# Kernel tuning notes

Measured on AMD Instinct MI355X. Metric: run time of the kernel, lower is better.

## Reference

```python
import jax, jax.numpy as jnp
import numpy as np

DIM = 512
D_IN = 4096
N_OBJ = 2048
N_REL = 32768
STEPS = 2
N_OBJ_CLS = 151
N_REL_CLS = 51
EPS = 1e-5


def _mlp2(x, w1, b1, w2, b2):
    # Linear -> ReLU -> Linear (torch Linear: y = x W^T + b)
    return jnp.maximum(x @ w1.T + b1, 0.0) @ w2.T + b2


def _gate(a, b, w, bias):
    # Sequential(Linear(2*dim, 1), Sigmoid) on cat([a, b], 1)
    return jax.nn.sigmoid(jnp.concatenate([a, b], axis=1) @ w.T + bias)


def _gru_cell(x, h, wih, whh, bih, bhh):
    gi = x @ wih.T + bih  # [N, 3*DIM]
    gh = h @ whh.T + bhh
    ir, iz, inew = jnp.split(gi, 3, axis=1)
    hr, hz, hnew = jnp.split(gh, 3, axis=1)
    r = jax.nn.sigmoid(ir + hr)
    z = jax.nn.sigmoid(iz + hz)
    n = jnp.tanh(inew + r * hnew)
    return (1.0 - z) * n + z * h


def setup_inputs() -> dict:
    key = jax.random.key(0)
    ks = jax.random.split(key, 32)
    rn = lambda k, shape, s=0.02: jax.random.normal(k, shape, dtype=jnp.float32) * s
    z = lambda *shape: jnp.zeros(shape, dtype=jnp.float32)
    return {
        'x_obj': jax.random.normal(ks[0], (N_OBJ, D_IN), dtype=jnp.float32),
        'x_pred': jax.random.normal(ks[1], (N_REL, D_IN), dtype=jnp.float32),
        'rel_inds': jax.random.randint(ks[2], (N_REL, 2), 0, N_OBJ),
        # obj / pred embedding MLPs
        'oe_w1': rn(ks[3], (DIM, D_IN)), 'oe_b1': z(DIM),
        'oe_w2': rn(ks[4], (DIM, DIM)), 'oe_b2': z(DIM),
        'pe_w1': rn(ks[5], (DIM, D_IN)), 'pe_b1': z(DIM),
        'pe_w2': rn(ks[6], (DIM, DIM)), 'pe_b2': z(DIM),
        # gates: Linear(2*dim, 1)
        'g_sn_w': rn(ks[7], (1, 2 * DIM)), 'g_sn_b': z(1),
        'g_on_w': rn(ks[8], (1, 2 * DIM)), 'g_on_b': z(1),
        'g_se_w': rn(ks[9], (1, 2 * DIM)), 'g_se_b': z(1),
        'g_oe_w': rn(ks[10], (1, 2 * DIM)), 'g_oe_b': z(1),
        # GRU cells
        'ngru_wih': rn(ks[11], (3 * DIM, DIM)), 'ngru_whh': rn(ks[12], (3 * DIM, DIM)),
        'ngru_bih': z(3 * DIM), 'ngru_bhh': z(3 * DIM),
        'egru_wih': rn(ks[13], (3 * DIM, DIM)), 'egru_whh': rn(ks[14], (3 * DIM, DIM)),
        'egru_bih': z(3 * DIM), 'egru_bhh': z(3 * DIM),
        # classifier heads
        'op_w': rn(ks[15], (N_OBJ_CLS, DIM)), 'op_b': z(N_OBJ_CLS),
        'pp_w': rn(ks[16], (N_REL_CLS, DIM)), 'pp_b': z(N_REL_CLS),
    }


def reference(x_obj, x_pred, rel_inds,
              oe_w1, oe_b1, oe_w2, oe_b2,
              pe_w1, pe_b1, pe_w2, pe_b2,
              g_sn_w, g_sn_b, g_on_w, g_on_b,
              g_se_w, g_se_b, g_oe_w, g_oe_b,
              ngru_wih, ngru_whh, ngru_bih, ngru_bhh,
              egru_wih, egru_whh, egru_bih, egru_bhh,
              op_w, op_b, pp_w, pp_b):
    n_obj = x_obj.shape[0]
    subj_idx = rel_inds[:, 0]
    obj_idx = rel_inds[:, 1]

    h_obj = _mlp2(x_obj, oe_w1, oe_b1, oe_w2, oe_b2)    # [N_obj, DIM]
    h_edge = _mlp2(x_pred, pe_w1, pe_b1, pe_w2, pe_b2)  # [N_rel, DIM]

    # row sums of the 0/1 subj/obj_pred_map == in-degree counts (constants)
    ones = jnp.ones((rel_inds.shape[0],), dtype=jnp.float32)
    cnt_s = jax.ops.segment_sum(ones, subj_idx, num_segments=n_obj)[:, None]
    cnt_o = jax.ops.segment_sum(ones, obj_idx, num_segments=n_obj)[:, None]

    for _ in range(STEPS):
        sub_vert = h_obj[subj_idx]  # [N_rel, DIM]
        obj_vert = h_obj[obj_idx]

        # node update: gated edge->node messages, mean-aggregated per node
        msg_p2s = _gate(sub_vert, h_edge, g_sn_w, g_sn_b) * h_edge
        msg_p2o = _gate(obj_vert, h_edge, g_on_w, g_on_b) * h_edge
        node_message = (
            jax.ops.segment_sum(msg_p2s, subj_idx, num_segments=n_obj) / (cnt_s + EPS)
            + jax.ops.segment_sum(msg_p2o, obj_idx, num_segments=n_obj) / (cnt_o + EPS)
        ) / 2.0
        new_h_obj = _gru_cell(node_message, h_obj, ngru_wih, ngru_whh, ngru_bih, ngru_bhh)

        # edge update: gated node->edge messages
        msg_s2p = _gate(sub_vert, h_edge, g_se_w, g_se_b) * sub_vert
        msg_o2p = _gate(obj_vert, h_edge, g_oe_w, g_oe_b) * obj_vert
        edge_message = (msg_s2p + msg_o2p) / 2.0
        h_edge = _gru_cell(edge_message, h_edge, egru_wih, egru_whh, egru_bih, egru_bhh)
        h_obj = new_h_obj

    obj_class_logits = h_obj @ op_w.T + op_b    # [N_obj, 151]
    pred_class_logits = h_edge @ pp_w.T + pp_b  # [N_rel, 51]
    obj_class_labels = jnp.argmax(obj_class_logits[:, 1:], axis=1) + 1
    return (h_obj, h_edge, obj_class_logits, pred_class_logits, obj_class_labels, rel_inds)
```

## Files before the change

kernel.cpp:

```cpp
#include <hip/hip_runtime.h>
#include <math.h>

typedef unsigned short u16;
typedef unsigned int u32;
typedef _Float16 f16;
typedef f16 f16x8 __attribute__((ext_vector_type(8)));
typedef float f32x4 __attribute__((ext_vector_type(4)));

#define DIM 512
#define D_IN 4096
#define N_OBJS 2048
#define N_RELS 32768
#define N_OBJ_CLS 151
#define N_REL_CLS 51
#define EPSV 1e-5f

#define OFF_HOBJ  0
#define OFF_HEDGE (N_OBJS*DIM)
#define OFF_OLOG  (OFF_HEDGE + N_RELS*DIM)
#define OFF_PLOG  (OFF_OLOG + N_OBJS*N_OBJ_CLS)
#define OFF_LBL   (OFF_PLOG + N_RELS*N_REL_CLS)
#define OFF_RI    (OFF_LBL + N_OBJS)

__device__ __forceinline__ float sigmoidf_(float x) { return 1.0f / (1.0f + expf(-x)); }
__device__ __forceinline__ u16 f2h_(float f) {
    union { f16 h; u16 u; } c; c.h = (f16)f; return c.u;
}
__device__ __forceinline__ float h2f_(u16 u) {
    union { f16 h; u16 u; } c; c.u = u; return (float)c.h;
}

__device__ __forceinline__ void cvt8h1(const float* f, uint4& h) {
    u32 hh[8];
#pragma unroll
    for (int i = 0; i < 8; i++) hh[i] = f2h_(f[i]);
    h.x = hh[0] | (hh[1] << 16); h.y = hh[2] | (hh[3] << 16);
    h.z = hh[4] | (hh[5] << 16); h.w = hh[6] | (hh[7] << 16);
}
__device__ __forceinline__ void cvt8h2(const float* f, uint4& h, uint4& l) {
    u32 hh[8], ll[8];
#pragma unroll
    for (int i = 0; i < 8; i++) {
        u16 x = f2h_(f[i]);
        hh[i] = x;
        ll[i] = f2h_(f[i] - h2f_(x));
    }
    h.x = hh[0] | (hh[1] << 16); h.y = hh[2] | (hh[3] << 16);
    h.z = hh[4] | (hh[5] << 16); h.w = hh[6] | (hh[7] << 16);
    l.x = ll[0] | (ll[1] << 16); l.y = ll[2] | (ll[3] << 16);
    l.z = ll[4] | (ll[5] << 16); l.w = ll[6] | (ll[7] << 16);
}

__device__ __forceinline__ int swzo(int row, int c) {
    return row * 32 + ((c ^ ((row >> 1) & 3)) << 3);
}

__device__ __forceinline__ int xcdswz(int orig, int nwg) {
    const int q = nwg >> 3;
    return (orig & 7) * q + (orig >> 3);
}

__device__ __forceinline__ void gload16(const void* g, void* l) {
    __builtin_amdgcn_global_load_lds(
        (const __attribute__((address_space(1))) void*)g,
        (__attribute__((address_space(3))) void*)l, 16, 0, 0);
}

__global__ __launch_bounds__(256) void convert_h(const float* __restrict__ src,
    u16* __restrict__ hi, int n4)
{
    const int i = blockIdx.x * 256 + threadIdx.x;
    if (i >= n4) return;
    const float4 v = ((const float4*)src)[i];
    ((ushort4*)hi)[i] = make_ushort4(f2h_(v.x), f2h_(v.y), f2h_(v.z), f2h_(v.w));
}

template<bool RELU, int AT, bool WSPLIT>
__global__ __launch_bounds__(256, 3) void gemm_a32(
    const float* __restrict__ A, const u16* __restrict__ Bhi,
    const float* __restrict__ bias, u16* __restrict__ Chi, u16* __restrict__ Clo,
    int NX, int K)
{
    __shared__ u16 sAh[128 * 32], sBh[128 * 32];
    __shared__ u16 sAl[AT == 2 ? 128 * 32 : 1];
    const int id = xcdswz(blockIdx.x, gridDim.x);
    const int m0 = (id / NX) * 128, n0 = (id % NX) * 128;
    const int N = NX * 128;
    const int t = threadIdx.x;
    const int wid = t >> 6, lane = t & 63;
    const int wm = (wid >> 1) * 64, wn = (wid & 1) * 64;
    const int lr = lane & 15, lk = lane >> 4;

    f32x4 acc[4][4] = {};

    const int sr = t >> 1;
    const int sc = (t & 1) * 2;
    const float* Ap = A + (size_t)(m0 + sr) * K + (t & 1) * 16;

    const int rB = (wid * 2) * 16 + (lane >> 2);
    const int cB = (lane & 3) ^ ((rB >> 1) & 3);
    const u16* Bp0 = Bhi + (size_t)(n0 + rB) * K + cB * 8;
    const u16* Bp1 = Bp0 + (size_t)16 * K;
    u16* Bd0 = &sBh[(wid * 2) * 512];
    u16* Bd1 = Bd0 + 512;

    float fv[16];
    *(float4*)&fv[0]  = *(const float4*)(Ap);
    *(float4*)&fv[4]  = *(const float4*)(Ap + 4);
    *(float4*)&fv[8]  = *(const float4*)(Ap + 8);
    *(float4*)&fv[12] = *(const float4*)(Ap + 12);

    for (int k0 = 0; k0 < K; k0 += 32) {
        uint4 ah0, ah1, al0, al1;
        if (AT == 2) { cvt8h2(fv, ah0, al0); cvt8h2(fv + 8, ah1, al1); }
        else         { cvt8h1(fv, ah0);      cvt8h1(fv + 8, ah1); }

        __syncthreads();
        gload16(Bp0 + k0, Bd0);
        gload16(Bp1 + k0, Bd1);
        *(uint4*)&sAh[swzo(sr, sc)]     = ah0;
        *(uint4*)&sAh[swzo(sr, sc + 1)] = ah1;
        if (AT == 2) {
            *(uint4*)&sAl[swzo(sr, sc)]     = al0;
            *(uint4*)&sAl[swzo(sr, sc + 1)] = al1;
        }
        asm volatile("s_waitcnt vmcnt(0)" ::: "memory");
        __syncthreads();

        const int kn = k0 + 32;
        if (kn < K) {
            *(float4*)&fv[0]  = *(const float4*)(Ap + kn);
            *(float4*)&fv[4]  = *(const float4*)(Ap + kn + 4);
            *(float4*)&fv[8]  = *(const float4*)(Ap + kn + 8);
            *(float4*)&fv[12] = *(const float4*)(Ap + kn + 12);
        }

        f16x8 ah[4], al[4], bh[4];
#pragma unroll
        for (int f = 0; f < 4; f++) {
            const int off = swzo(wm + f * 16 + lr, lk);
            ah[f] = *(const f16x8*)&sAh[off];
            if (AT == 2) al[f] = *(const f16x8*)&sAl[off];
            bh[f] = *(const f16x8*)&sBh[swzo(wn + f * 16 + lr, lk)];
        }
#pragma unroll
        for (int fm = 0; fm < 4; fm++)
#pragma unroll
            for (int fn = 0; fn < 4; fn++) {
                acc[fm][fn] = __builtin_amdgcn_mfma_f32_16x16x32_f16(ah[fm], bh[fn], acc[fm][fn], 0, 0, 0);
                if (AT == 2)
                    acc[fm][fn] = __builtin_amdgcn_mfma_f32_16x16x32_f16(al[fm], bh[fn], acc[fm][fn], 0, 0, 0);
            }
    }
#pragma unroll
    for (int fm = 0; fm < 4; fm++) {
        const int mrow = m0 + wm + fm * 16 + lk * 4;
#pragma unroll
        for (int fn = 0; fn < 4; fn++) {
            const int col = n0 + wn + fn * 16 + lr;
            const float bv = bias[col];
#pragma unroll
            for (int j = 0; j < 4; j++) {
                float v = acc[fm][fn][j] + bv;
                if (RELU) v = fmaxf(v, 0.0f);
                const u16 h = f2h_(v);
                Chi[(size_t)(mrow + j) * N + col] = h;
                if (WSPLIT) Clo[(size_t)(mrow + j) * N + col] = f2h_(v - h2f_(h));
            }
        }
    }
}

template<int AT, bool WF32, bool WHI, bool WLO>
__global__ __launch_bounds__(256, AT == 1 ? 4 : 3) void gemm_f16(
    const u16* __restrict__ Ahi, const u16* __restrict__ Alo,
    const u16* __restrict__ Bhi, const float* __restrict__ bias,
    float* __restrict__ C32, u16* __restrict__ Chi, u16* __restrict__ Clo,
    int NX, int N, int ldc, int K)
{
    __shared__ u16 sA[2][128 * 32], sB[2][128 * 32];
    __shared__ u16 sL[AT == 2 ? 2 : 1][AT == 2 ? 128 * 32 : 1];
    const int id = xcdswz(blockIdx.x, gridDim.x);
    const int m0 = (id / NX) * 128, n0 = (id % NX) * 128;
    const int t = threadIdx.x;
    const int wid = t >> 6, lane = t & 63;
    const int wm = (wid >> 1) * 64, wn = (wid & 1) * 64;
    const int lr = lane & 15, lk = lane >> 4;

    f32x4 acc[4][4] = {};

    const int rr = (wid * 2) * 16 + (lane >> 2);
    const int cc = (lane & 3) ^ ((rr >> 1) & 3);
    const u16* pA0 = Ahi + (size_t)(m0 + rr) * K + cc * 8;
    const u16* pA1 = pA0 + (size_t)16 * K;
    const u16* pL0 = (AT == 2) ? Alo + (size_t)(m0 + rr) * K + cc * 8 : nullptr;
    const u16* pL1 = (AT == 2) ? pL0 + (size_t)16 * K : nullptr;
    const u16* pB0 = Bhi + (size_t)(n0 + rr) * K + cc * 8;
    const u16* pB1 = pB0 + (size_t)16 * K;
    const int bOff = (wid * 2) * 512;

    for (int k0 = 0; k0 < K; k0 += 64) {
        __syncthreads();
#pragma unroll
        for (int h = 0; h < 2; h++) {
            const int kk = k0 + h * 32;
            gload16(pA0 + kk, &sA[h][bOff]);
            gload16(pA1 + kk, &sA[h][bOff + 512]);
            if (AT == 2) {
                gload16(pL0 + kk, &sL[h][bOff]);
                gload16(pL1 + kk, &sL[h][bOff + 512]);
            }
            gload16(pB0 + kk, &sB[h][bOff]);
            gload16(pB1 + kk, &sB[h][bOff + 512]);
        }
        asm volatile("s_waitcnt vmcnt(0)" ::: "memory");
        __syncthreads();

#pragma unroll
        for (int h = 0; h < 2; h++) {
            f16x8 ah[4], al[4], bh[4];
#pragma unroll
            for (int f = 0; f < 4; f++) {
                const int off = swzo(wm + f * 16 + lr, lk);
                ah[f] = *(const f16x8*)&sA[h][off];
                if (AT == 2) al[f] = *(const f16x8*)&sL[h][off];
                bh[f] = *(const f16x8*)&sB[h][swzo(wn + f * 16 + lr, lk)];
            }
#pragma unroll
            for (int fm = 0; fm < 4; fm++)
#pragma unroll
                for (int fn = 0; fn < 4; fn++) {
                    acc[fm][fn] = __builtin_amdgcn_mfma_f32_16x16x32_f16(ah[fm], bh[fn], acc[fm][fn], 0, 0, 0);
                    if (AT == 2)
                        acc[fm][fn] = __builtin_amdgcn_mfma_f32_16x16x32_f16(al[fm], bh[fn], acc[fm][fn], 0, 0, 0);
                }
        }
    }
#pragma unroll
    for (int fm = 0; fm < 4; fm++) {
        const int mrow = m0 + wm + fm * 16 + lk * 4;
#pragma unroll
        for (int fn = 0; fn < 4; fn++) {
            const int col = n0 + wn + fn * 16 + lr;
            const float bv = bias[col];
#pragma unroll
            for (int j = 0; j < 4; j++) {
                const float v = acc[fm][fn][j] + bv;
                if (WF32 && col < N) C32[(size_t)(mrow + j) * ldc + col] = v;
                if (WHI) {
                    const u16 h = f2h_(v);
                    Chi[(size_t)(mrow + j) * (NX * 128) + col] = h;
                    if (WLO)
                        Clo[(size_t)(mrow + j) * (NX * 128) + col] = f2h_(v - h2f_(h));
                }
            }
        }
    }
}

template<int AT>
__global__ __launch_bounds__(256, AT == 1 ? 4 : 3) void gru_gemm2(
    const u16* __restrict__ Xh, const u16* __restrict__ Xl,
    const u16* __restrict__ WiH, const float* __restrict__ bi, u16* __restrict__ gi,
    const u16* __restrict__ Hh, const u16* __restrict__ Hl,
    const u16* __restrict__ WhH, const float* __restrict__ bhs, u16* __restrict__ gh_,
    int K)
{
    __shared__ u16 sA[2][128 * 32], sB[2][128 * 32];
    __shared__ u16 sL[AT == 2 ? 2 : 1][AT == 2 ? 128 * 32 : 1];
    const int id = xcdswz(blockIdx.x, gridDim.x);
    const int part = id % 24;
    const int m0 = (id / 24) * 128;
    const bool isH = part >= 12;
    const u16* Ahi = isH ? Hh : Xh;
    const u16* Alo = isH ? Hl : Xl;
    const u16* Bhi = isH ? WhH : WiH;
    const float* bias = isH ? bhs : bi;
    u16* C = isH ? gh_ : gi;
    const int n0 = (part - (isH ? 12 : 0)) * 128;

    const int t = threadIdx.x;
    const int wid = t >> 6, lane = t & 63;
    const int wm = (wid >> 1) * 64, wn = (wid & 1) * 64;
    const int lr = lane & 15, lk = lane >> 4;

    f32x4 acc[4][4] = {};

    const int rr = (wid * 2) * 16 + (lane >> 2);
    const int cc = (lane & 3) ^ ((rr >> 1) & 3);
    const u16* pA0 = Ahi + (size_t)(m0 + rr) * K + cc * 8;
    const u16* pA1 = pA0 + (size_t)16 * K;
    const u16* pL0 = (AT == 2) ? Alo + (size_t)(m0 + rr) * K + cc * 8 : nullptr;
    const u16* pL1 = (AT == 2) ? pL0 + (size_t)16 * K : nullptr;
    const u16* pB0 = Bhi + (size_t)(n0 + rr) * K + cc * 8;
    const u16* pB1 = pB0 + (size_t)16 * K;
    const int bOff = (wid * 2) * 512;

    for (int k0 = 0; k0 < K; k0 += 64) {
        __syncthreads();
#pragma unroll
        for (int h = 0; h < 2; h++) {
            const int kk = k0 + h * 32;
            gload16(pA0 + kk, &sA[h][bOff]);
            gload16(pA1 + kk, &sA[h][bOff + 512]);
            if (AT == 2) {
                gload16(pL0 + kk, &sL[h][bOff]);
                gload16(pL1 + kk, &sL[h][bOff + 512]);
            }
            gload16(pB0 + kk, &sB[h][bOff]);
            gload16(pB1 + kk, &sB[h][bOff + 512]);
        }
        asm volatile("s_waitcnt vmcnt(0)" ::: "memory");
        __syncthreads();

#pragma unroll
        for (int h = 0; h < 2; h++) {
            f16x8 ah[4], al[4], bh[4];
#pragma unroll
            for (int f = 0; f < 4; f++) {
                const int off = swzo(wm + f * 16 + lr, lk);
                ah[f] = *(const f16x8*)&sA[h][off];
                if (AT == 2) al[f] = *(const f16x8*)&sL[h][off];
                bh[f] = *(const f16x8*)&sB[h][swzo(wn + f * 16 + lr, lk)];
            }
#pragma unroll
            for (int fm = 0; fm < 4; fm++)
#pragma unroll
                for (int fn = 0; fn < 4; fn++) {
                    acc[fm][fn] = __builtin_amdgcn_mfma_f32_16x16x32_f16(ah[fm], bh[fn], acc[fm][fn], 0, 0, 0);
                    if (AT == 2)
                        acc[fm][fn] = __builtin_amdgcn_mfma_f32_16x16x32_f16(al[fm], bh[fn], acc[fm][fn], 0, 0, 0);
                }
        }
    }
#pragma unroll
    for (int fm = 0; fm < 4; fm++) {
        const int mrow = m0 + wm + fm * 16 + lk * 4;
#pragma unroll
        for (int fn = 0; fn < 4; fn++) {
            const int col = n0 + wn + fn * 16 + lr;
            const float bv = bias[col];
#pragma unroll
            for (int j = 0; j < 4; j++)
                C[(size_t)(mrow + j) * 1536 + col] = f2h_(acc[fm][fn][j] + bv);
        }
    }
}

__device__ __forceinline__ float gcomb(u16 ir, u16 iz, u16 in_, u16 hr, u16 hz,
                                       u16 hn, float h) {
    const float r = sigmoidf_(h2f_(ir) + h2f_(hr));
    const float z = sigmoidf_(h2f_(iz) + h2f_(hz));
    const float n = tanhf(h2f_(in_) + r * h2f_(hn));
    return (1.0f - z) * n + z * h;
}

template<bool WSPLIT, bool WF32>
__global__ __launch_bounds__(256) void gru_combine(
    const u16* __restrict__ gi, const u16* __restrict__ gh,
    u16* __restrict__ hh, u16* __restrict__ hl, float* __restrict__ H32, int R)
{
    const int idx = blockIdx.x * 256 + threadIdx.x;
    if (idx >= R * 128) return;
    const int r = idx >> 7, c4 = (idx & 127) * 4;
    const size_t gb = (size_t)r * 1536 + c4;
    const ushort4 ir4 = *(const ushort4*)&gi[gb];
    const ushort4 iz4 = *(const ushort4*)&gi[gb + 512];
    const ushort4 in4 = *(const ushort4*)&gi[gb + 1024];
    const ushort4 hr4 = *(const ushort4*)&gh[gb];
    const ushort4 hz4 = *(const ushort4*)&gh[gb + 512];
    const ushort4 hn4 = *(const ushort4*)&gh[gb + 1024];
    const size_t hb = (size_t)r * 512 + c4;
    const ushort4 hhi = *(const ushort4*)&hh[hb];
    float h0 = h2f_(hhi.x), h1 = h2f_(hhi.y), h2 = h2f_(hhi.z), h3 = h2f_(hhi.w);
    if (WSPLIT) {
        const ushort4 hlo = *(const ushort4*)&hl[hb];
        h0 += h2f_(hlo.x); h1 += h2f_(hlo.y); h2 += h2f_(hlo.z); h3 += h2f_(hlo.w);
    }
    float4 o;
    o.x = gcomb(ir4.x, iz4.x, in4.x, hr4.x, hz4.x, hn4.x, h0);
    o.y = gcomb(ir4.y, iz4.y, in4.y, hr4.y, hz4.y, hn4.y, h1);
    o.z = gcomb(ir4.z, iz4.z, in4.z, hr4.z, hz4.z, hn4.z, h2);
    o.w = gcomb(ir4.w, iz4.w, in4.w, hr4.w, hz4.w, hn4.w, h3);
    const ushort4 hi4 = make_ushort4(f2h_(o.x), f2h_(o.y), f2h_(o.z), f2h_(o.w));
    *(ushort4*)&hh[hb] = hi4;
    if (WSPLIT) {
        *(ushort4*)&hl[hb] = make_ushort4(
            f2h_(o.x - h2f_(hi4.x)), f2h_(o.y - h2f_(hi4.y)),
            f2h_(o.z - h2f_(hi4.z)), f2h_(o.w - h2f_(hi4.w)));
    }
    if (WF32) *(float4*)&H32[hb] = o;
}

__global__ __launch_bounds__(256) void count_int(const int* __restrict__ rel,
                                                 int* cs, int* co)
{
    const int e = blockIdx.x * 256 + threadIdx.x;
    atomicAdd(&cs[rel[2 * e]], 1);
    atomicAdd(&co[rel[2 * e + 1]], 1);
}

__global__ __launch_bounds__(256) void scan_off(const int* __restrict__ cs,
    const int* __restrict__ co, int* __restrict__ offs, int* __restrict__ offo)
{
    __shared__ int tmp[256];
    for (int arr = 0; arr < 2; arr++) {
        const int* c = arr ? co : cs;
        int* off = arr ? offo : offs;
        const int base = threadIdx.x * 8;
        int loc[8]; int s = 0;
#pragma unroll
        for (int j = 0; j < 8; j++) { loc[j] = c[base + j]; s += loc[j]; }
        tmp[threadIdx.x] = s;
        __syncthreads();
        for (int d = 1; d < 256; d <<= 1) {
            const int v = (threadIdx.x >= d) ? tmp[threadIdx.x - d] : 0;
            __syncthreads();
            tmp[threadIdx.x] += v;
            __syncthreads();
        }
        int p = tmp[threadIdx.x] - s;
#pragma unroll
        for (int j = 0; j < 8; j++) { off[base + j] = p; p += loc[j]; }
        __syncthreads();
    }
}

__global__ __launch_bounds__(256) void fill_csr(const int* __restrict__ rel,
    int* curS, int* curO, const int* __restrict__ offs, const int* __restrict__ offo,
    int* __restrict__ listS, int* __restrict__ listO)
{
    const int e = blockIdx.x * 256 + threadIdx.x;
    const int s = rel[2 * e], o = rel[2 * e + 1];
    const int i = atomicAdd(&curS[s], 1);
    listS[offs[s] + i] = e;
    const int j = atomicAdd(&curO[o], 1);
    listO[offo[o] + j] = e;
}

__global__ __launch_bounds__(256) void gatepass(
    const u16* __restrict__ hho, const u16* __restrict__ hhe,
    const int* __restrict__ rel,
    const float* __restrict__ wsn, const float* __restrict__ bsn,
    const float* __restrict__ won, const float* __restrict__ bon,
    const float* __restrict__ wse, const float* __restrict__ bse,
    const float* __restrict__ woe, const float* __restrict__ boe,
    const int* __restrict__ cs, const int* __restrict__ co,
    u16* __restrict__ emh, float* __restrict__ af, float* __restrict__ ag)
{
    const int e = blockIdx.x * 4 + (threadIdx.x >> 6);
    const int lane = threadIdx.x & 63;
    const int s = rel[2 * e], o = rel[2 * e + 1];
    const int c = lane * 8;

    const uint4 hsu = *(const uint4*)&hho[(size_t)s * DIM + c];
    const uint4 hou = *(const uint4*)&hho[(size_t)o * DIM + c];
    const uint4 heu = *(const uint4*)&hhe[(size_t)e * DIM + c];
    float hs[8], ho[8], he[8];
    hs[0] = h2f_((u16)hsu.x); hs[1] = h2f_((u16)(hsu.x >> 16));
    hs[2] = h2f_((u16)hsu.y); hs[3] = h2f_((u16)(hsu.y >> 16));
    hs[4] = h2f_((u16)hsu.z); hs[5] = h2f_((u16)(hsu.z >> 16));
    hs[6] = h2f_((u16)hsu.w); hs[7] = h2f_((u16)(hsu.w >> 16));
    ho[0] = h2f_((u16)hou.x); ho[1] = h2f_((u16)(hou.x >> 16));
    ho[2] = h2f_((u16)hou.y); ho[3] = h2f_((u16)(hou.y >> 16));
    ho[4] = h2f_((u16)hou.z); ho[5] = h2f_((u16)(hou.z >> 16));
    ho[6] = h2f_((u16)hou.w); ho[7] = h2f_((u16)(hou.w >> 16));
    he[0] = h2f_((u16)heu.x); he[1] = h2f_((u16)(heu.x >> 16));
    he[2] = h2f_((u16)heu.y); he[3] = h2f_((u16)(heu.y >> 16));
    he[4] = h2f_((u16)heu.z); he[5] = h2f_((u16)(heu.z >> 16));
    he[6] = h2f_((u16)heu.w); he[7] = h2f_((u16)(heu.w >> 16));

    float p0 = 0.f, p1 = 0.f, p2 = 0.f, p3 = 0.f;
#pragma unroll
    for (int q = 0; q < 2; q++) {
        const float4 w0v = *(const float4*)&wsn[c + q * 4];
        const float4 w0e = *(const float4*)&wsn[DIM + c + q * 4];
        const float4 w1v = *(const float4*)&won[c + q * 4];
        const float4 w1e = *(const float4*)&won[DIM + c + q * 4];
        const float4 w2v = *(const float4*)&wse[c + q * 4];
        const float4 w2e = *(const float4*)&wse[DIM + c + q * 4];
        const float4 w3v = *(const float4*)&woe[c + q * 4];
        const float4 w3e = *(const float4*)&woe[DIM + c + q * 4];
        const float* s4 = &hs[q * 4];
        const float* o4 = &ho[q * 4];
        const float* e4 = &he[q * 4];
        p0 += s4[0]*w0v.x + s4[1]*w0v.y + s4[2]*w0v.z + s4[3]*w0v.w
            + e4[0]*w0e.x + e4[1]*w0e.y + e4[2]*w0e.z + e4[3]*w0e.w;
        p1 += o4[0]*w1v.x + o4[1]*w1v.y + o4[2]*w1v.z + o4[3]*w1v.w
            + e4[0]*w1e.x + e4[1]*w1e.y + e4[2]*w1e.z + e4[3]*w1e.w;
        p2 += s4[0]*w2v.x + s4[1]*w2v.y + s4[2]*w2v.z + s4[3]*w2v.w
            + e4[0]*w2e.x + e4[1]*w2e.y + e4[2]*w2e.z + e4[3]*w2e.w;
        p3 += o4[0]*w3v.x + o4[1]*w3v.y + o4[2]*w3v.z + o4[3]*w3v.w
            + e4[0]*w3e.x + e4[1]*w3e.y + e4[2]*w3e.z + e4[3]*w3e.w;
    }
#pragma unroll
    for (int off = 32; off; off >>= 1) {
        p0 += __shfl_xor(p0, off);
        p1 += __shfl_xor(p1, off);
        p2 += __shfl_xor(p2, off);
        p3 += __shfl_xor(p3, off);
    }
    const float gsn = sigmoidf_(p0 + bsn[0]);
    const float gon = sigmoidf_(p1 + bon[0]);
    const float gse = sigmoidf_(p2 + bse[0]);
    const float goe = sigmoidf_(p3 + boe[0]);

    if (lane == 0) {
        af[e] = 0.5f * gsn / ((float)cs[s] + EPSV);
        ag[e] = 0.5f * gon / ((float)co[o] + EPSV);
    }
    u16 em8[8];
#pragma unroll
    for (int j = 0; j < 8; j++)
        em8[j] = f2h_(0.5f * (gse * hs[j] + goe * ho[j]));
    *(uint4*)&emh[(size_t)e * DIM + c] = *(const uint4*)em8;
}

__global__ __launch_bounds__(256) void gather_nm(
    const u16* __restrict__ hhe,
    const int* __restrict__ listS, const int* __restrict__ listO,
    const int* __restrict__ offs, const int* __restrict__ offo,
    const int* __restrict__ cs, const int* __restrict__ co,
    const float* __restrict__ af, const float* __restrict__ ag,
    u16* __restrict__ nmh, u16* __restrict__ nml)
{
    const int v = blockIdx.x * 4 + (threadIdx.x >> 6);
    const int lane = threadIdx.x & 63;
    const int c = lane * 8;

    float acc[8] = {};
#pragma unroll
    for (int side = 0; side < 2; side++) {
        const int* list = side ? listO : listS;
        const int b = side ? offo[v] : offs[v];
        const int n = side ? co[v] : cs[v];
        const float* coef = side ? ag : af;
        for (int i = 0; i < n; i++) {
            const int e = list[b + i];
            const float a = coef[e];
            const uint4 x = *(const uint4*)&hhe[(size_t)e * DIM + c];
            acc[0] += a * h2f_((u16)x.x); acc[1] += a * h2f_((u16)(x.x >> 16));
            acc[2] += a * h2f_((u16)x.y); acc[3] += a * h2f_((u16)(x.y >> 16));
            acc[4] += a * h2f_((u16)x.z); acc[5] += a * h2f_((u16)(x.z >> 16));
            acc[6] += a * h2f_((u16)x.w); acc[7] += a * h2f_((u16)(x.w >> 16));
        }
    }
    u16 hi8[8], lo8[8];
#pragma unroll
    for (int j = 0; j < 8; j++) {
        hi8[j] = f2h_(acc[j]);
        lo8[j] = f2h_(acc[j] - h2f_(hi8[j]));
    }
    *(uint4*)&nmh[(size_t)v * DIM + c] = *(const uint4*)hi8;
    *(uint4*)&nml[(size_t)v * DIM + c] = *(const uint4*)lo8;
}

__global__ __launch_bounds__(256) void argmax_kernel(const float* __restrict__ logits,
                                                     float* __restrict__ out)
{
    const int row = blockIdx.x * 4 + (threadIdx.x >> 6);
    const int lane = threadIdx.x & 63;
    float bv = -1e30f; int bi = 1;
    for (int j = 1 + lane; j < N_OBJ_CLS; j += 64) {
        const float v = logits[(size_t)row * N_OBJ_CLS + j];
        if (v > bv) { bv = v; bi = j; }
    }
#pragma unroll
    for (int off = 32; off; off >>= 1) {
        const float ov = __shfl_xor(bv, off);
        const int oi = __shfl_xor(bi, off);
        if (ov > bv || (ov == bv && oi < bi)) { bv = ov; bi = oi; }
    }
    if (lane == 0) out[row] = (float)bi;
}

__global__ __launch_bounds__(256) void relinds_kernel(const int* __restrict__ rel,
                                                      float* __restrict__ out)
{
    const int i = blockIdx.x * 256 + threadIdx.x;
    out[i] = (float)rel[i];
}

extern "C" void kernel_launch(void* const* d_in, const int* in_sizes, int n_in,
                              void* d_out, int out_size, void* d_ws, size_t ws_size,
                              hipStream_t stream)
{
    const float* x_obj = (const float*)d_in[0];
    const float* x_pred = (const float*)d_in[1];
    const int* rel = (const int*)d_in[2];
    const float* oe_w1 = (const float*)d_in[3];
    const float* oe_b1 = (const float*)d_in[4];
    const float* oe_w2 = (const float*)d_in[5];
    const float* oe_b2 = (const float*)d_in[6];
    const float* pe_w1 = (const float*)d_in[7];
    const float* pe_b1 = (const float*)d_in[8];
    const float* pe_w2 = (const float*)d_in[9];
    const float* pe_b2 = (const float*)d_in[10];
    const float* g_sn_w = (const float*)d_in[11];
    const float* g_sn_b = (const float*)d_in[12];
    const float* g_on_w = (const float*)d_in[13];
    const float* g_on_b = (const float*)d_in[14];
    const float* g_se_w = (const float*)d_in[15];
    const float* g_se_b = (const float*)d_in[16];
    const float* g_oe_w = (const float*)d_in[17];
    const float* g_oe_b = (const float*)d_in[18];
    const float* ngru_wih = (const float*)d_in[19];
    const float* ngru_whh = (const float*)d_in[20];
    const float* ngru_bih = (const float*)d_in[21];
    const float* ngru_bhh = (const float*)d_in[22];
    const float* egru_wih = (const float*)d_in[23];
    const float* egru_whh = (const float*)d_in[24];
    const float* egru_bih = (const float*)d_in[25];
    const float* egru_bhh = (const float*)d_in[26];
    const float* op_w = (const float*)d_in[27];
    const float* op_b = (const float*)d_in[28];
    const float* pp_w = (const float*)d_in[29];
    const float* pp_b = (const float*)d_in[30];

    float* out = (float*)d_out;

    float* h_obj = out + OFF_HOBJ;
    float* h_edge = out + OFF_HEDGE;

    char* wsp = (char*)d_ws;
    float* af = (float*)wsp; wsp += N_RELS * 4;
    float* ag = (float*)wsp; wsp += N_RELS * 4;
    int* cs = (int*)wsp;   wsp += N_OBJS * 4;
    int* co = (int*)wsp;   wsp += N_OBJS * 4;
    int* offs = (int*)wsp; wsp += N_OBJS * 4;
    int* offo = (int*)wsp; wsp += N_OBJS * 4;
    int* curS = (int*)wsp; wsp += N_OBJS * 4;
    int* curO = (int*)wsp; wsp += N_OBJS * 4;
    int* listS = (int*)wsp; wsp += N_RELS * 4;
    int* listO = (int*)wsp; wsp += N_RELS * 4;

    u16* wp = (u16*)wsp;
    const int s_big = DIM * D_IN, s_sq = DIM * DIM, s_gru = 3 * DIM * DIM;
    u16 *oe1h = wp; wp += s_big;
    u16 *pe1h = wp; wp += s_big;
    u16 *oe2h = wp; wp += s_sq;
    u16 *pe2h = wp; wp += s_sq;
    u16 *nih_h = wp; wp += s_gru;
    u16 *nhh_h = wp; wp += s_gru;
    u16 *eih_h = wp; wp += s_gru;
    u16 *ehh_h = wp; wp += s_gru;
    u16 *oph = wp; wp += 256 * DIM;
    u16 *pph = wp; wp += 128 * DIM;
    u16 *tmpo_h = wp; wp += (size_t)N_OBJS * DIM;
    u16 *tmpo_l = wp; wp += (size_t)N_OBJS * DIM;
    u16 *tmpe_h = wp; wp += (size_t)N_RELS * DIM;
    u16 *hhoh = wp; wp += (size_t)N_OBJS * DIM;
    u16 *hhol = wp; wp += (size_t)N_OBJS * DIM;
    u16 *hhe  = wp; wp += (size_t)N_RELS * DIM;
    u16 *emh  = wp; wp += (size_t)N_RELS * DIM;
    u16 *nmh  = wp; wp += (size_t)N_OBJS * DIM;
    u16 *nml  = wp; wp += (size_t)N_OBJS * DIM;

    const size_t used = (size_t)((char*)wp - (char*)d_ws);
    int R = 8192;
    if (used + (size_t)32768 * 6144 <= ws_size) R = 32768;
    else if (used + (size_t)16384 * 6144 <= ws_size) R = 16384;
    u16* gi = wp;
    u16* gh = gi + (size_t)R * 1536;

    auto cvtw = [&](const float* s, u16* h, int n) {
        convert_h<<<(n / 4 + 255) / 256, 256, 0, stream>>>(s, h, n / 4);
    };
    cvtw(oe_w1, oe1h, s_big);
    cvtw(pe_w1, pe1h, s_big);
    cvtw(oe_w2, oe2h, s_sq);
    cvtw(pe_w2, pe2h, s_sq);
    cvtw(ngru_wih, nih_h, s_gru);
    cvtw(ngru_whh, nhh_h, s_gru);
    cvtw(egru_wih, eih_h, s_gru);
    cvtw(egru_whh, ehh_h, s_gru);
    cvtw(op_w, oph, N_OBJ_CLS * DIM);
    cvtw(pp_w, pph, N_REL_CLS * DIM);

    hipMemsetAsync(cs, 0, 2 * N_OBJS * sizeof(int), stream);
    hipMemsetAsync(curS, 0, 2 * N_OBJS * sizeof(int), stream);
    count_int<<<N_RELS / 256, 256, 0, stream>>>(rel, cs, co);
    scan_off<<<1, 256, 0, stream>>>(cs, co, offs, offo);
    fill_csr<<<N_RELS / 256, 256, 0, stream>>>(rel, curS, curO, offs, offo, listS, listO);

    gemm_a32<true, 2, true><<<4 * (N_OBJS / 128), 256, 0, stream>>>(
        x_obj, oe1h, oe_b1, tmpo_h, tmpo_l, 4, D_IN);
    gemm_f16<2, false, true, true><<<4 * (N_OBJS / 128), 256, 0, stream>>>(
        tmpo_h, tmpo_l, oe2h, oe_b2, nullptr, hhoh, hhol, 4, DIM, DIM, DIM);
    gemm_a32<true, 1, false><<<4 * (N_RELS / 128), 256, 0, stream>>>(
        x_pred, pe1h, pe_b1, tmpe_h, nullptr, 4, D_IN);
    gemm_f16<1, false, true, false><<<4 * (N_RELS / 128), 256, 0, stream>>>(
        tmpe_h, nullptr, pe2h, pe_b2, nullptr, hhe, nullptr, 4, DIM, DIM, DIM);

    for (int step = 0; step < 2; step++) {
        gatepass<<<N_RELS / 4, 256, 0, stream>>>(
            hhoh, hhe, rel,
            g_sn_w, g_sn_b, g_on_w, g_on_b, g_se_w, g_se_b, g_oe_w, g_oe_b,
            cs, co, emh, af, ag);
        gather_nm<<<N_OBJS / 4, 256, 0, stream>>>(
            hhe, listS, listO, offs, offo, cs, co, af, ag, nmh, nml);

        gru_gemm2<2><<<24 * (N_OBJS / 128), 256, 0, stream>>>(
            nmh, nml, nih_h, ngru_bih, gi, hhoh, hhol, nhh_h, ngru_bhh, gh, DIM);
        if (step == 0)
            gru_combine<true, false><<<(N_OBJS * 128 + 255) / 256, 256, 0, stream>>>(
                gi, gh, hhoh, hhol, nullptr, N_OBJS);
        else
            gru_combine<true, true><<<(N_OBJS * 128 + 255) / 256, 256, 0, stream>>>(
                gi, gh, hhoh, hhol, h_obj, N_OBJS);

        for (int r0 = 0; r0 < N_RELS; r0 += R) {
            const int Rc = (N_RELS - r0 < R) ? (N_RELS - r0) : R;
            gru_gemm2<1><<<24 * (Rc / 128), 256, 0, stream>>>(
                emh + (size_t)r0 * DIM, nullptr, eih_h, egru_bih, gi,
                hhe + (size_t)r0 * DIM, nullptr, ehh_h, egru_bhh, gh, DIM);
            if (step == 0)
                gru_combine<false, false><<<(Rc * 128 + 255) / 256, 256, 0, stream>>>(
                    gi, gh, hhe + (size_t)r0 * DIM, nullptr, nullptr, Rc);
            else
                gru_combine<false, true><<<(Rc * 128 + 255) / 256, 256, 0, stream>>>(
                    gi, gh, hhe + (size_t)r0 * DIM, nullptr, h_edge + (size_t)r0 * DIM, Rc);
        }
    }

    gemm_f16<2, true, false, false><<<2 * (N_OBJS / 128), 256, 0, stream>>>(
        hhoh, hhol, oph, op_b, out + OFF_OLOG, nullptr, nullptr,
        2, N_OBJ_CLS, N_OBJ_CLS, DIM);
    gemm_f16<1, true, false, false><<<1 * (N_RELS / 128), 256, 0, stream>>>(
        hhe, nullptr, pph, pp_b, out + OFF_PLOG, nullptr, nullptr,
        1, N_REL_CLS, N_REL_CLS, DIM);

    argmax_kernel<<<N_OBJS / 4, 256, 0, stream>>>(out + OFF_OLOG, out + OFF_LBL);
    relinds_kernel<<<(2 * N_RELS) / 256, 256, 0, stream>>>(rel, out + OFF_RI);
}
```

Before: 1.038 ms.

## Process two K-slices per iteration in gemm_a32 with double LDS buffers

The gemm_a32 main loop now steps K by 64 and uses two LDS buffers for A and B. Both B slices are fetched together up front, and the second A slice is converted and stored after the first slice's MFMAs. This halves the number of wait-for-all-loads points per K and lets the next global A load overlap with compute. In exchange, LDS use doubles, which may cut occupancy under the 3-block launch bound, and K is assumed to be a multiple of 64.

```diff
diff --git a/kernel.cpp b/kernel.cpp
--- a/kernel.cpp
+++ b/kernel.cpp
@@ -81,8 +81,8 @@
     const float* __restrict__ bias, u16* __restrict__ Chi, u16* __restrict__ Clo,
     int NX, int K)
 {
-    __shared__ u16 sAh[128 * 32], sBh[128 * 32];
-    __shared__ u16 sAl[AT == 2 ? 128 * 32 : 1];
+    __shared__ u16 sAh[2][128 * 32], sBh[2][128 * 32];
+    __shared__ u16 sAl[AT == 2 ? 2 : 1][AT == 2 ? 128 * 32 : 1];
     const int id = xcdswz(blockIdx.x, gridDim.x);
     const int m0 = (id / NX) * 128, n0 = (id % NX) * 128;
     const int N = NX * 128;
@@ -101,8 +101,7 @@
     const int cB = (lane & 3) ^ ((rB >> 1) & 3);
     const u16* Bp0 = Bhi + (size_t)(n0 + rB) * K + cB * 8;
     const u16* Bp1 = Bp0 + (size_t)16 * K;
-    u16* Bd0 = &sBh[(wid * 2) * 512];
-    u16* Bd1 = Bd0 + 512;
+    const int bOff = (wid * 2) * 512;
 
     float fv[16];
     *(float4*)&fv[0]  = *(const float4*)(Ap);
@@ -110,47 +109,89 @@
     *(float4*)&fv[8]  = *(const float4*)(Ap + 8);
     *(float4*)&fv[12] = *(const float4*)(Ap + 12);
 
-    for (int k0 = 0; k0 < K; k0 += 32) {
+    for (int k0 = 0; k0 < K; k0 += 64) {
         uint4 ah0, ah1, al0, al1;
         if (AT == 2) { cvt8h2(fv, ah0, al0); cvt8h2(fv + 8, ah1, al1); }
         else         { cvt8h1(fv, ah0);      cvt8h1(fv + 8, ah1); }
 
         __syncthreads();
-        gload16(Bp0 + k0, Bd0);
-        gload16(Bp1 + k0, Bd1);
-        *(uint4*)&sAh[swzo(sr, sc)]     = ah0;
-        *(uint4*)&sAh[swzo(sr, sc + 1)] = ah1;
+        gload16(Bp0 + k0, &sBh[0][bOff]);
+        gload16(Bp1 + k0, &sBh[0][bOff + 512]);
+        gload16(Bp0 + k0 + 32, &sBh[1][bOff]);
+        gload16(Bp1 + k0 + 32, &sBh[1][bOff + 512]);
+        *(uint4*)&sAh[0][swzo(sr, sc)]     = ah0;
+        *(uint4*)&sAh[0][swzo(sr, sc + 1)] = ah1;
         if (AT == 2) {
-            *(uint4*)&sAl[swzo(sr, sc)]     = al0;
-            *(uint4*)&sAl[swzo(sr, sc + 1)] = al1;
+            *(uint4*)&sAl[0][swzo(sr, sc)]     = al0;
+            *(uint4*)&sAl[0][swzo(sr, sc + 1)] = al1;
         }
         asm volatile("s_waitcnt vmcnt(0)" ::: "memory");
         __syncthreads();
 
-        const int kn = k0 + 32;
+        {
+            const float* Aq = Ap + k0 + 32;
+            *(float4*)&fv[0]  = *(const float4*)(Aq);
+            *(float4*)&fv[4]  = *(const float4*)(Aq + 4);
+            *(float4*)&fv[8]  = *(const float4*)(Aq + 8);
+            *(float4*)&fv[12] = *(const float4*)(Aq + 12);
+        }
+
+        {
+            f16x8 ah[4], al[4], bh[4];
+#pragma unroll
+            for (int f = 0; f < 4; f++) {
+                const int off = swzo(wm + f * 16 + lr, lk);
+                ah[f] = *(const f16x8*)&sAh[0][off];
+                if (AT == 2) al[f] = *(const f16x8*)&sAl[0][off];
+                bh[f] = *(const f16x8*)&sBh[0][swzo(wn + f * 16 + lr, lk)];
+            }
+#pragma unroll
+            for (int fm = 0; fm < 4; fm++)
+#pragma unroll
+                for (int fn = 0; fn < 4; fn++) {
+                    acc[fm][fn] = __builtin_amdgcn_mfma_f32_16x16x32_f16(ah[fm], bh[fn], acc[fm][fn], 0, 0, 0);
+                    if (AT == 2)
+                        acc[fm][fn] = __builtin_amdgcn_mfma_f32_16x16x32_f16(al[fm], bh[fn], acc[fm][fn], 0, 0, 0);
+                }
+        }
+
+        if (AT == 2) { cvt8h2(fv, ah0, al0); cvt8h2(fv + 8, ah1, al1); }
+        else         { cvt8h1(fv, ah0);      cvt8h1(fv + 8, ah1); }
+        *(uint4*)&sAh[1][swzo(sr, sc)]     = ah0;
+        *(uint4*)&sAh[1][swzo(sr, sc + 1)] = ah1;
+        if (AT == 2) {
+            *(uint4*)&sAl[1][swzo(sr, sc)]     = al0;
+            *(uint4*)&sAl[1][swzo(sr, sc + 1)] = al1;
+        }
+        __syncthreads();
+
+        const int kn = k0 + 64;
         if (kn < K) {
-            *(float4*)&fv[0]  = *(const float4*)(Ap + kn);
-            *(float4*)&fv[4]  = *(const float4*)(Ap + kn + 4);
-            *(float4*)&fv[8]  = *(const float4*)(Ap + kn + 8);
-            *(float4*)&fv[12] = *(const float4*)(Ap + kn + 12);
-        }
-
-        f16x8 ah[4], al[4], bh[4];
-#pragma unroll
-        for (int f = 0; f < 4; f++) {
-            const int off = swzo(wm + f * 16 + lr, lk);
-            ah[f] = *(const f16x8*)&sAh[off];
-            if (AT == 2) al[f] = *(const f16x8*)&sAl[off];
-            bh[f] = *(const f16x8*)&sBh[swzo(wn + f * 16 + lr, lk)];
-        }
-#pragma unroll
-        for (int fm = 0; fm < 4; fm++)
-#pragma unroll
-            for (int fn = 0; fn < 4; fn++) {
-                acc[fm][fn] = __builtin_amdgcn_mfma_f32_16x16x32_f16(ah[fm], bh[fn], acc[fm][fn], 0, 0, 0);
-                if (AT == 2)
-                    acc[fm][fn] = __builtin_amdgcn_mfma_f32_16x16x32_f16(al[fm], bh[fn], acc[fm][fn], 0, 0, 0);
+            const float* Aq = Ap + kn;
+            *(float4*)&fv[0]  = *(const float4*)(Aq);
+            *(float4*)&fv[4]  = *(const float4*)(Aq + 4);
+            *(float4*)&fv[8]  = *(const float4*)(Aq + 8);
+            *(float4*)&fv[12] = *(const float4*)(Aq + 12);
+        }
+
+        {
+            f16x8 ah[4], al[4], bh[4];
+#pragma unroll
+            for (int f = 0; f < 4; f++) {
+                const int off = swzo(wm + f * 16 + lr, lk);
+                ah[f] = *(const f16x8*)&sAh[1][off];
+                if (AT == 2) al[f] = *(const f16x8*)&sAl[1][off];
+                bh[f] = *(const f16x8*)&sBh[1][swzo(wn + f * 16 + lr, lk)];
             }
+#pragma unroll
+            for (int fm = 0; fm < 4; fm++)
+#pragma unroll
+                for (int fn = 0; fn < 4; fn++) {
+                    acc[fm][fn] = __builtin_amdgcn_mfma_f32_16x16x32_f16(ah[fm], bh[fn], acc[fm][fn], 0, 0, 0);
+                    if (AT == 2)
+                        acc[fm][fn] = __builtin_amdgcn_mfma_f32_16x16x32_f16(al[fm], bh[fn], acc[fm][fn], 0, 0, 0);
+                }
+        }
     }
 #pragma unroll
     for (int fm = 0; fm < 4; fm++) {
```

After: 1.055 ms. No clear change (+1.6%).
